# Performance work log

Measured on AMD Instinct MI355X. Metric: run time of the kernel, lower is better.

## Reference

```python
import jax, jax.numpy as jnp
import numpy as np

EMBD_SIZE = 128
NUM_HEADS = 8
HEAD_SIZE = 16

def setup_inputs() -> dict:
    key = jax.random.key(0)
    ks = jax.random.split(key, 6)
    B, S = 8, 2048
    x = jax.random.normal(ks[0], (B, S, EMBD_SIZE), dtype=jnp.float32)
    # per-head Linear weights, torch layout [out, in] stacked over heads -> [H, hs, E]
    sc = 1.0 / np.sqrt(EMBD_SIZE)
    Wk = jax.random.normal(ks[1], (NUM_HEADS, HEAD_SIZE, EMBD_SIZE), dtype=jnp.float32) * sc
    Wq = jax.random.normal(ks[2], (NUM_HEADS, HEAD_SIZE, EMBD_SIZE), dtype=jnp.float32) * sc
    Wv = jax.random.normal(ks[3], (NUM_HEADS, HEAD_SIZE, EMBD_SIZE), dtype=jnp.float32) * sc
    Wp = jax.random.normal(ks[4], (EMBD_SIZE, NUM_HEADS * HEAD_SIZE), dtype=jnp.float32) * sc
    bp = jax.random.normal(ks[5], (EMBD_SIZE,), dtype=jnp.float32) * 0.01
    return {"x": x, "Wk": Wk, "Wq": Wq, "Wv": Wv, "Wp": Wp, "bp": bp}

def reference(x, Wk, Wq, Wv, Wp, bp):
    # x: [B,S,E]; W{k,q,v}: [H,hs,E]; Wp: [E,H*hs]
    B, S, E = x.shape
    H, hs, _ = Wk.shape
    q = jnp.einsum('bse,hde->bhsd', x, Wq)
    k = jnp.einsum('bse,hde->bhsd', x, Wk)
    v = jnp.einsum('bse,hde->bhsd', x, Wv)
    # NOTE: original code MULTIPLIES by sqrt(head_size) (k.shape[-1]**0.5)
    scores = jnp.einsum('bhsd,bhtd->bhst', q, k) * (hs ** 0.5)
    wei = jax.nn.softmax(scores, axis=-1)  # dropout is identity in eval mode
    out = jnp.einsum('bhst,bhtd->bhsd', wei, v)
    # concat heads along last dim: [B,S,H*hs]
    out = out.transpose(0, 2, 1, 3).reshape(B, S, H * hs)
    return out @ Wp.T + bp
```

## Files before the change

### kernel.cpp

```cpp
#include <hip/hip_runtime.h>
#include <hip/hip_bf16.h>

constexpr int Bb  = 8;
constexpr int Ss  = 2048;
constexpr int Ee  = 128;
constexpr int Hh  = 8;
constexpr int HSs = 16;
constexpr int QKVSZ = Bb * Hh * Ss * HSs;

typedef _Float16 f16;
typedef __attribute__((ext_vector_type(8)))  _Float16 f16x8;
typedef __attribute__((ext_vector_type(16))) float f32x16;

constexpr float QSCALE = 5.770780163555854f;

__device__ __forceinline__ unsigned pack_rtz(float lo, float hi) {
    union { __fp16 __attribute__((ext_vector_type(2))) h; unsigned u; } c;
    c.h = __builtin_amdgcn_cvt_pkrtz(lo, hi);
    return c.u;
}
__device__ __forceinline__ unsigned pack_rne(float lo, float hi) {
    union { __attribute__((ext_vector_type(2))) _Float16 h; unsigned u; } c;
    c.h[0] = (f16)lo; c.h[1] = (f16)hi;
    return c.u;
}

__device__ __forceinline__ float vmax16(const f32x16& v) {
    float a = fmaxf(fmaxf(v[0],  v[1]),  v[2]);
    float b = fmaxf(fmaxf(v[3],  v[4]),  v[5]);
    float c = fmaxf(fmaxf(v[6],  v[7]),  v[8]);
    float d = fmaxf(fmaxf(v[9],  v[10]), v[11]);
    float e = fmaxf(fmaxf(v[12], v[13]), v[14]);
    float g = fmaxf(fmaxf(a, b), c);
    float h = fmaxf(fmaxf(d, e), v[15]);
    return fmaxf(g, h);
}

__device__ __forceinline__ f16x8 cvt8(const float4& w0, const float4& w1) {
    union { f16x8 v; unsigned u[4]; } wf;
    wf.u[0] = pack_rne(w0.x, w0.y); wf.u[1] = pack_rne(w0.z, w0.w);
    wf.u[2] = pack_rne(w1.x, w1.y); wf.u[3] = pack_rne(w1.z, w1.w);
    return wf.v;
}

__global__ __launch_bounds__(512, 4) void qkv_kernel(
    const float* __restrict__ x,
    const float* __restrict__ Wq, const float* __restrict__ Wk,
    const float* __restrict__ Wv,
    f16* __restrict__ qo, f16* __restrict__ ko, f16* __restrict__ vo)
{
    constexpr int LDW = 136;
    __shared__ __align__(16) f16 Xs[32 * LDW];

    const int rowbase = blockIdx.x * 32;

    for (int idx = threadIdx.x; idx < 32 * 32; idx += 512) {
        const int r = idx >> 5, cp = idx & 31;
        float4 v = *(const float4*)(x + (size_t)(rowbase + r) * Ee + cp * 4);
        union { f16 h[4]; uint2 u; } cv;
        cv.h[0] = (f16)v.x; cv.h[1] = (f16)v.y; cv.h[2] = (f16)v.z; cv.h[3] = (f16)v.w;
        *(uint2*)&Xs[r * LDW + cp * 4] = cv.u;
    }
    __syncthreads();

    const int wid = threadIdx.x >> 6, lane = threadIdx.x & 63;
    const int h = lane >> 5, n31 = lane & 31;

    f16x8 Xf[8];
#pragma unroll
    for (int t = 0; t < 8; ++t)
        Xf[t] = *(const f16x8*)&Xs[n31 * LDW + 16 * t + 8 * h];

    const int b = rowbase >> 11;
    const int s0 = rowbase & 2047;

    if (wid < 4) {
        const int s = s0 + n31;
#pragma unroll
        for (int mat = 0; mat < 2; ++mat) {
            const float* W = (mat == 0) ? Wq : Wk;
            const float* wr32 = W + (size_t)(wid * 32 + n31) * Ee + 8 * h;
            f32x16 acc = {};
#pragma unroll
            for (int t = 0; t < 8; ++t) {
                float4 w0 = *(const float4*)(wr32 + 16 * t);
                float4 w1 = *(const float4*)(wr32 + 16 * t + 4);
                acc = __builtin_amdgcn_mfma_f32_32x32x16_f16(cvt8(w0, w1), Xf[t], acc, 0, 0, 0);
            }
            f16* dst = (mat == 0) ? qo : ko;
            const float scale = (mat == 1) ? QSCALE : 1.f;
#pragma unroll
            for (int rq = 0; rq < 4; ++rq) {
                const int cbase = wid * 32 + 8 * rq + 4 * h;
                const int head = cbase >> 4, dbase = cbase & 15;
                union { f16 hv[4]; uint2 u; } pk4;
#pragma unroll
                for (int i = 0; i < 4; ++i) pk4.hv[i] = (f16)(acc[4 * rq + i] * scale);
                *(uint2*)(dst + ((size_t)(b * Hh + head) * Ss + s) * HSs + dbase) = pk4.u;
            }
        }
    } else {
        const int g = wid - 4;
        const int c = g * 32 + n31;
        const int head = c >> 4, d = c & 15;
        const int bh = b * Hh + head;
        const int it = s0 >> 6, g0 = (s0 >> 4) & 3;
        const float* wr32 = Wv + (size_t)c * Ee + 8 * h;
        f32x16 acc = {};
#pragma unroll
        for (int t = 0; t < 8; ++t) {
            float4 w0 = *(const float4*)(wr32 + 16 * t);
            float4 w1 = *(const float4*)(wr32 + 16 * t + 4);
            acc = __builtin_amdgcn_mfma_f32_32x32x16_f16(Xf[t], cvt8(w0, w1), acc, 0, 0, 0);
        }
        f16* vb = vo + (size_t)bh * 65536 + it * 2048;
#pragma unroll
        for (int rq = 0; rq < 4; ++rq) {
            union { f16 hv[4]; uint2 u; } pk4;
#pragma unroll
            for (int i = 0; i < 4; ++i) pk4.hv[i] = (f16)acc[4 * rq + i];
            *(uint2*)(vb + (g0 + (rq >> 1)) * 512 + (d + 32 * h) * 8 + 4 * (rq & 1)) = pk4.u;
        }

        for (int i = threadIdx.x - 256; i < 512; i += 256) {
            const int gp = i >> 8, hd = (i >> 5) & 7, cc = i & 31;
            const int lanep = (cc < 16) ? 16 + cc : 32 + cc;
            const unsigned one2 = 0x3C003C00u;
            uint4 val = ((cc & 15) == 0) ? (uint4){one2, one2, one2, one2}
                                         : (uint4){0, 0, 0, 0};
            *(uint4*)(vo + (size_t)(b * Hh + hd) * 65536 + it * 2048
                      + (g0 + gp) * 512 + lanep * 8) = val;
        }
    }
}

__global__ __launch_bounds__(512, 4) void attn_kernel(
    const f16* __restrict__ qg, const f16* __restrict__ kg,
    const f16* __restrict__ vg, const float* __restrict__ wp32,
    const float* __restrict__ bp, float* __restrict__ out)
{
    constexpr int LDW = 136;
    __shared__ __align__(16) f16 Os[32 * LDW];

    const int b    = blockIdx.x & 7;
    const int qblk = blockIdx.x >> 3;
    const int wid  = threadIdx.x >> 6;
    const int lane = threadIdx.x & 63;
    const int h    = lane >> 5;
    const int q31  = lane & 31;
    const int qbase = qblk * 32;
    const int bh   = b * Hh + wid;

    const f16x8 qf = *(const f16x8*)(qg + ((size_t)bh * Ss + qbase + q31) * HSs + 8 * h);

    const f16* pk = kg + (size_t)bh * Ss * HSs + q31 * 16 + 8 * h;
    const f16* pv = vg + (size_t)bh * 65536 + lane * 8;

    f16x8 ka = *(const f16x8*)pk;

    f32x16 acc = {};
    f32x16 cinit = {};

    constexpr int NCH = Ss / 32;
    for (int c = 0; c < NCH; ++c) {
        const f16* pvc = pv + (size_t)c * 1024;
        f16x8 va0 = *(const f16x8*)(pvc);
        f16x8 va1 = *(const f16x8*)(pvc + 512);

        f32x16 st = __builtin_amdgcn_mfma_f32_32x32x16_f16(ka, qf, cinit, 0, 0, 0);

        if (c + 1 < NCH) ka = *(const f16x8*)(pk + (c + 1) * 512);

        float mx = vmax16(st);
        mx = fmaxf(mx, __shfl_xor(mx, 32, 64));

        if (__any(mx > 8.f)) {
            const float delta = fmaxf(mx, 0.f);
            const float corr  = __builtin_amdgcn_exp2f(-delta);
#pragma unroll
            for (int r = 0; r < 9; ++r) acc[r] *= corr;
#pragma unroll
            for (int t = 0; t < 16; ++t) st[t] -= delta;
#pragma unroll
            for (int r = 0; r < 16; ++r) cinit[r] -= delta;
        }

        {
            union { unsigned u[4]; f16x8 v; } B;
#pragma unroll
            for (int r = 0; r < 4; ++r)
                B.u[r] = pack_rtz(__builtin_amdgcn_exp2f(st[2 * r]),
                                  __builtin_amdgcn_exp2f(st[2 * r + 1]));
            __builtin_amdgcn_s_setprio(1);
            acc = __builtin_amdgcn_mfma_f32_32x32x16_f16(va0, B.v, acc, 0, 0, 0);
            __builtin_amdgcn_s_setprio(0);
        }
        {
            union { unsigned u[4]; f16x8 v; } B;
#pragma unroll
            for (int r = 0; r < 4; ++r)
                B.u[r] = pack_rtz(__builtin_amdgcn_exp2f(st[8 + 2 * r]),
                                  __builtin_amdgcn_exp2f(st[9 + 2 * r]));
            __builtin_amdgcn_s_setprio(1);
            acc = __builtin_amdgcn_mfma_f32_32x32x16_f16(va1, B.v, acc, 0, 0, 0);
            __builtin_amdgcn_s_setprio(0);
        }
    }

    const float l = acc[8] + __shfl_xor(acc[8], 32, 64);
    const float inv = 1.f / l;

    f16* orow = &Os[q31 * LDW + wid * HSs + 4 * h];
    uint2 lo = { pack_rne(acc[0] * inv, acc[1] * inv), pack_rne(acc[2] * inv, acc[3] * inv) };
    uint2 hi = { pack_rne(acc[4] * inv, acc[5] * inv), pack_rne(acc[6] * inv, acc[7] * inv) };
    *(uint2*)(orow)     = lo;
    *(uint2*)(orow + 8) = hi;
    __syncthreads();

    if (wid >= 4) return;

    f16x8 A[8];
#pragma unroll
    for (int t = 0; t < 8; ++t)
        A[t] = *(const f16x8*)&Os[q31 * LDW + 16 * t + 8 * h];

    const int e = wid * 32 + q31;
    const float* wr32 = wp32 + (size_t)e * Ee + 8 * h;
    f32x16 acc2 = {};
#pragma unroll
    for (int t = 0; t < 8; ++t) {
        float4 w0 = *(const float4*)(wr32 + 16 * t);
        float4 w1 = *(const float4*)(wr32 + 16 * t + 4);
        acc2 = __builtin_amdgcn_mfma_f32_32x32x16_f16(A[t], cvt8(w0, w1), acc2, 0, 0, 0);
    }

    const float bias = bp[e];
#pragma unroll
    for (int r = 0; r < 16; ++r) {
        const int R = qbase + (r & 3) + 8 * (r >> 2) + 4 * h;
        out[((size_t)b * Ss + R) * Ee + e] = acc2[r] + bias;
    }
}

extern "C" void kernel_launch(void* const* d_in, const int* in_sizes, int n_in,
                              void* d_out, int out_size, void* d_ws, size_t ws_size,
                              hipStream_t stream)
{
    const float* x  = (const float*)d_in[0];
    const float* Wk = (const float*)d_in[1];
    const float* Wq = (const float*)d_in[2];
    const float* Wv = (const float*)d_in[3];
    const float* Wp = (const float*)d_in[4];
    const float* bp = (const float*)d_in[5];
    float* out = (float*)d_out;

    f16* ws = (f16*)d_ws;
    f16* qh = ws;
    f16* kh = ws + (size_t)QKVSZ;
    f16* vh = ws + (size_t)2 * QKVSZ;

    qkv_kernel<<<Bb * Ss / 32, 512, 0, stream>>>(x, Wq, Wk, Wv, qh, kh, vh);
    attn_kernel<<<Bb * Ss / 32, 512, 0, stream>>>(qh, kh, vh, Wp, bp, out);
}
```

Baseline: 133.7 us.

## Software-pipeline QK^T MFMA one chunk ahead of softmax and PV

Restructures the attention inner loop into a two-stage software pipeline unrolled by two. The score MFMA and row max for chunk c+1 are issued while the exp/pack work and PV MFMAs for chunk c run, and K/V loads are prefetched a chunk further ahead. The goal is to hide MFMA latency and the max-reduction dependency that serialized each iteration. The cost is more live registers, one wasted score MFMA on the last step, and prefetch loads that read past the end of each head's K/V range.

```diff
diff --git a/kernel.cpp b/kernel.cpp
--- a/kernel.cpp
+++ b/kernel.cpp
@@ -134,6 +134,48 @@
     }
 }
 
+__device__ __forceinline__ void chunk_step(
+    f32x16& stC, float& mxC, f32x16& stN, float& mxN,
+    const f16x8 kaN, const f16x8 vaC0, const f16x8 vaC1,
+    f16x8& kaN2, f16x8& vaN0, f16x8& vaN1,
+    const f16* __restrict__ pkN2, const f16* __restrict__ pvN,
+    f32x16& acc, f32x16& cinit, const f16x8 qf)
+{
+    if (__any(mxC > 8.f)) {
+        const float delta = fmaxf(mxC, 0.f);
+        const float corr  = __builtin_amdgcn_exp2f(-delta);
+#pragma unroll
+        for (int r = 0; r < 9; ++r) acc[r] *= corr;
+#pragma unroll
+        for (int t = 0; t < 16; ++t) stC[t] -= delta;
+#pragma unroll
+        for (int r = 0; r < 16; ++r) cinit[r] -= delta;
+    }
+
+    stN = __builtin_amdgcn_mfma_f32_32x32x16_f16(kaN, qf, cinit, 0, 0, 0);
+
+    kaN2 = *(const f16x8*)pkN2;
+    vaN0 = *(const f16x8*)(pvN);
+    vaN1 = *(const f16x8*)(pvN + 512);
+
+    union { unsigned u[4]; f16x8 v; } B0, B1;
+#pragma unroll
+    for (int r = 0; r < 4; ++r)
+        B0.u[r] = pack_rtz(__builtin_amdgcn_exp2f(stC[2 * r]),
+                           __builtin_amdgcn_exp2f(stC[2 * r + 1]));
+#pragma unroll
+    for (int r = 0; r < 4; ++r)
+        B1.u[r] = pack_rtz(__builtin_amdgcn_exp2f(stC[8 + 2 * r]),
+                           __builtin_amdgcn_exp2f(stC[9 + 2 * r]));
+    __builtin_amdgcn_s_setprio(1);
+    acc = __builtin_amdgcn_mfma_f32_32x32x16_f16(vaC0, B0.v, acc, 0, 0, 0);
+    acc = __builtin_amdgcn_mfma_f32_32x32x16_f16(vaC1, B1.v, acc, 0, 0, 0);
+    __builtin_amdgcn_s_setprio(0);
+
+    float m16 = vmax16(stN);
+    mxN = fmaxf(m16, __shfl_xor(m16, 32, 64));
+}
+
 __global__ __launch_bounds__(512, 4) void attn_kernel(
     const f16* __restrict__ qg, const f16* __restrict__ kg,
     const f16* __restrict__ vg, const float* __restrict__ wp32,
@@ -156,55 +198,33 @@
     const f16* pk = kg + (size_t)bh * Ss * HSs + q31 * 16 + 8 * h;
     const f16* pv = vg + (size_t)bh * 65536 + lane * 8;
 
-    f16x8 ka = *(const f16x8*)pk;
-
     f32x16 acc = {};
     f32x16 cinit = {};
 
+    f32x16 stA, stB;
+    float mxA, mxB;
+    f16x8 kaN, kaN2, vaC0, vaC1, vaN0, vaN1;
+
+    {
+        f16x8 ka0 = *(const f16x8*)pk;
+        kaN  = *(const f16x8*)(pk + 512);
+        vaC0 = *(const f16x8*)(pv);
+        vaC1 = *(const f16x8*)(pv + 512);
+        stA  = __builtin_amdgcn_mfma_f32_32x32x16_f16(ka0, qf, cinit, 0, 0, 0);
+        float m16 = vmax16(stA);
+        mxA = fmaxf(m16, __shfl_xor(m16, 32, 64));
+    }
+
     constexpr int NCH = Ss / 32;
-    for (int c = 0; c < NCH; ++c) {
-        const f16* pvc = pv + (size_t)c * 1024;
-        f16x8 va0 = *(const f16x8*)(pvc);
-        f16x8 va1 = *(const f16x8*)(pvc + 512);
-
-        f32x16 st = __builtin_amdgcn_mfma_f32_32x32x16_f16(ka, qf, cinit, 0, 0, 0);
-
-        if (c + 1 < NCH) ka = *(const f16x8*)(pk + (c + 1) * 512);
-
-        float mx = vmax16(st);
-        mx = fmaxf(mx, __shfl_xor(mx, 32, 64));
-
-        if (__any(mx > 8.f)) {
-            const float delta = fmaxf(mx, 0.f);
-            const float corr  = __builtin_amdgcn_exp2f(-delta);
-#pragma unroll
-            for (int r = 0; r < 9; ++r) acc[r] *= corr;
-#pragma unroll
-            for (int t = 0; t < 16; ++t) st[t] -= delta;
-#pragma unroll
-            for (int r = 0; r < 16; ++r) cinit[r] -= delta;
-        }
-
-        {
-            union { unsigned u[4]; f16x8 v; } B;
-#pragma unroll
-            for (int r = 0; r < 4; ++r)
-                B.u[r] = pack_rtz(__builtin_amdgcn_exp2f(st[2 * r]),
-                                  __builtin_amdgcn_exp2f(st[2 * r + 1]));
-            __builtin_amdgcn_s_setprio(1);
-            acc = __builtin_amdgcn_mfma_f32_32x32x16_f16(va0, B.v, acc, 0, 0, 0);
-            __builtin_amdgcn_s_setprio(0);
-        }
-        {
-            union { unsigned u[4]; f16x8 v; } B;
-#pragma unroll
-            for (int r = 0; r < 4; ++r)
-                B.u[r] = pack_rtz(__builtin_amdgcn_exp2f(st[8 + 2 * r]),
-                                  __builtin_amdgcn_exp2f(st[9 + 2 * r]));
-            __builtin_amdgcn_s_setprio(1);
-            acc = __builtin_amdgcn_mfma_f32_32x32x16_f16(va1, B.v, acc, 0, 0, 0);
-            __builtin_amdgcn_s_setprio(0);
-        }
+    for (int c = 0; c < NCH; c += 2) {
+        chunk_step(stA, mxA, stB, mxB, kaN, vaC0, vaC1,
+                   kaN2, vaN0, vaN1,
+                   pk + (size_t)(c + 2) * 512, pv + (size_t)(c + 1) * 1024,
+                   acc, cinit, qf);
+        chunk_step(stB, mxB, stA, mxA, kaN2, vaN0, vaN1,
+                   kaN, vaC0, vaC1,
+                   pk + (size_t)(c + 3) * 512, pv + (size_t)(c + 2) * 1024,
+                   acc, cinit, qf);
     }
 
     const float l = acc[8] + __shfl_xor(acc[8], 32, 64);
```

Result: no change. 132.2 us (-1.1%).
